# Kernel tuning notes

Hardware: AMD Instinct MI355X
Metric: run time of the kernel (lower is better)

## Reference

```python
import jax, jax.numpy as jnp
import numpy as np
from jax import lax

BOS, EOS = 62, 63
NEG_BIG = -10000.0


def setup_inputs() -> dict:
    key = jax.random.key(0)
    k_em, k_tag, k_len, k_tr = jax.random.split(key, 4)
    B, S, L = 512, 1024, 64
    emissions = jax.random.normal(k_em, (B, S, L), dtype=jnp.float32)
    tags = jax.random.randint(k_tag, (B, S), 0, 62).astype(jnp.int64)
    # valid-prefix mask from random lengths in [S//2, S]
    lengths = jax.random.randint(k_len, (B,), S // 2, S + 1)
    mask = (jnp.arange(S)[None, :] < lengths[:, None]).astype(jnp.float32)
    # transitions: uniform(-0.1, 0.1) with BOS/EOS constraints as in init_weights
    transitions = jax.random.uniform(k_tr, (L, L), minval=-0.1, maxval=0.1, dtype=jnp.float32)
    transitions = transitions.at[:, BOS].set(NEG_BIG)
    transitions = transitions.at[EOS, :].set(NEG_BIG)
    return {"emissions": emissions, "tags": tags, "mask": mask, "transitions": transitions}


def _crf_nll(emissions, tags, mask, transitions):
    B, S, L = emissions.shape
    # ----- gold-path scores -----
    first_tags = tags[:, 0]
    last_idx = (mask.sum(axis=1).astype(jnp.int32) - 1)  # (B,)
    last_tags = jnp.take_along_axis(tags, last_idx[:, None].astype(tags.dtype), axis=1)[:, 0]
    scores = transitions[BOS, first_tags]
    scores = scores + jnp.take_along_axis(emissions[:, 0], first_tags[:, None], axis=1)[:, 0]
    prev_t, cur_t = tags[:, :-1], tags[:, 1:]
    e_step = jnp.take_along_axis(emissions[:, 1:], cur_t[..., None], axis=-1)[..., 0]  # (B,S-1)
    t_step = transitions[prev_t, cur_t]  # (B,S-1)
    scores = scores + jnp.sum((e_step + t_step) * mask[:, 1:], axis=1)
    scores = scores + transitions[last_tags, EOS]
    # ----- log-partition via forward algorithm -----
    alpha0 = transitions[BOS][None, :] + emissions[:, 0]  # (B,L)
    em_t = jnp.moveaxis(emissions[:, 1:], 1, 0)  # (S-1,B,L)
    mk_t = mask[:, 1:].T  # (S-1,B)

    def step(alpha, xs):
        e_t, m_t = xs
        # alpha[b,i] + T[i,j] + e_t[b,j] -> logsumexp over i
        new = jax.nn.logsumexp(alpha[:, :, None] + transitions[None, :, :] + e_t[:, None, :], axis=1)
        return jnp.where(m_t[:, None] > 0, new, alpha), None

    alpha, _ = lax.scan(step, alpha0, (em_t, mk_t))
    partition = jax.nn.logsumexp(alpha + transitions[:, EOS][None, :], axis=1)  # (B,)
    return -jnp.sum(scores - partition)


def reference(emissions, tags, mask, transitions):
    return _crf_nll(emissions, tags, mask, transitions)
```

## Files before the change

kernel.cpp:

```cpp
#include <hip/hip_runtime.h>
#include <math.h>

#define BOS_TAG 62
#define EOS_TAG 63
#define S_LEN   1024
#define NCH     32
#define CH      32
#define WPB     2
#define LN2F    0.69314718055994530942f

typedef short  short8 __attribute__((ext_vector_type(8)));
typedef float  f32x4  __attribute__((ext_vector_type(4)));

template <int CTRL>
__device__ __forceinline__ int dpp_mov(int v) {
  return __builtin_amdgcn_update_dpp(v, v, CTRL, 0xf, 0xf, false);
}
template <int CTRL>
__device__ __forceinline__ float dpp_fmax_step(float v) {
  return fmaxf(v, __int_as_float(dpp_mov<CTRL>(__float_as_int(v))));
}
__device__ __forceinline__ float wave_fmax_all(float v) {
  v = dpp_fmax_step<0x111>(v); v = dpp_fmax_step<0x112>(v);
  v = dpp_fmax_step<0x114>(v); v = dpp_fmax_step<0x118>(v);
  v = dpp_fmax_step<0x142>(v); v = dpp_fmax_step<0x143>(v);
  return __int_as_float(__builtin_amdgcn_readlane(__float_as_int(v), 63));
}
template <int CTRL>
__device__ __forceinline__ float dpp_fadd_step(float v) {
  int t = __builtin_amdgcn_update_dpp(0, __float_as_int(v), CTRL, 0xf, 0xf, true);
  return v + __int_as_float(t);
}
__device__ __forceinline__ float wave_sum_all(float v) {
  v = dpp_fadd_step<0x111>(v); v = dpp_fadd_step<0x112>(v);
  v = dpp_fadd_step<0x114>(v); v = dpp_fadd_step<0x118>(v);
  v = dpp_fadd_step<0x142>(v); v = dpp_fadd_step<0x143>(v);
  return __int_as_float(__builtin_amdgcn_readlane(__float_as_int(v), 63));
}
__device__ __forceinline__ unsigned short f2bf(float v) {
  return (unsigned short)((__float_as_uint(v) + 0x8000u) >> 16);
}
__device__ __forceinline__ float bf2f(unsigned short u) {
  return __uint_as_float(((unsigned)u) << 16);
}

__global__ __launch_bounds__(256) void crf_lens(
    const float* __restrict__ mask, int* __restrict__ lens, int B)
{
  const int b = blockIdx.x * 4 + (threadIdx.x >> 6);
  if (b >= B) return;
  const int l = threadIdx.x & 63;
  const float4* mb = (const float4*)(mask + (size_t)b * S_LEN);
  float s = 0.f;
#pragma unroll
  for (int i = 0; i < 4; ++i) { float4 q = mb[l + 64 * i]; s += q.x + q.y + q.z + q.w; }
  s = wave_sum_all(s);
  if (l == 0) lens[b] = max(1, min(S_LEN, (int)(s + 0.5f)));
}

__global__ __launch_bounds__(256) void crf_ptab(
    const float* __restrict__ trans, short8* __restrict__ pfrag,
    float* __restrict__ tvf)
{
  const int tid = threadIdx.x;
  for (int e = tid; e < 1024; e += 256) {
    int lane = e & 63, kc = (e >> 6) & 1, m = (e >> 7) & 3, dir = e >> 9;
    int g = lane >> 4, c = lane & 15;
    int out = 16 * m + c;
    short8 f;
#pragma unroll
    for (int j = 0; j < 8; ++j) {
      int in = 16 * (2 * kc + (j >> 2)) + 4 * g + (j & 3);
      float tv = dir ? trans[out * 64 + in] : trans[in * 64 + out];
      f[j] = (short)f2bf(__expf(tv));
    }
    pfrag[e] = f;
  }
  if (tid < 64) tvf[tid] = __expf(trans[tid * 64 + EOS_TAG]);
}

__global__ __launch_bounds__(256, 2) void crf_chunk_mfma(
    const float* __restrict__ em, const float* __restrict__ trans,
    const int* __restrict__ lens, const short8* __restrict__ pfrag,
    unsigned short* __restrict__ Vf, unsigned short* __restrict__ Vb,
    float* __restrict__ sf, float* __restrict__ sb,
    float* __restrict__ m0a, int B)
{
  const int l  = threadIdx.x & 63;
  const int w  = blockIdx.x * 4 + (threadIdx.x >> 6);
  const int nwaves = 2 * B * WPB;
  if (w >= nwaves) return;
  const int dir  = w & 1;
  const int idx  = w >> 1;
  const int b    = idx / WPB;
  const int half = idx % WPB;
  const float* embase = em + (size_t)b * S_LEN * 64;
  const int g = l >> 4, c = l & 15;

  const int len = lens[b];

  float m0 = 0.f;
  if (dir == 0 && half == 0) {
    float a0 = trans[BOS_TAG * 64 + l] + embase[l];
    m0 = wave_fmax_all(a0);
    if (l == 0) m0a[b] = m0;
  }

  unsigned short* Vout = dir ? Vb : Vf;
  float* sout = dir ? sb : sf;
  int ps = -1, pr = -1;
#pragma unroll
  for (int r = 0; r < 16; ++r) {
    int kg = half * 16 + r;
    int fs = min((kg + 1) * CH, len - 1) - (kg * CH + 1);
    if (fs < 0) {
      Vout[((size_t)b * NCH + kg) * 64 + l] = 0x3F80;
      if (l == 0) sout[b * NCH + kg] = 0.f;
    }
    if (fs >= 0 && fs < CH - 1) { ps = fs; pr = r; }
  }

  if (half * 16 * CH + 1 > len - 1) return;

  short8 Af[4][2];
#pragma unroll
  for (int m = 0; m < 4; ++m)
#pragma unroll
    for (int kc = 0; kc < 2; ++kc)
      Af[m][kc] = pfrag[((dir * 4 + m) * 2 + kc) * 64 + l];

  float d[4][4];
#pragma unroll
  for (int m = 0; m < 4; ++m)
#pragma unroll
    for (int r = 0; r < 4; ++r) d[m][r] = 1.0f;
  if (dir == 0 && half == 0 && c == 0) {
#pragma unroll
    for (int m = 0; m < 4; ++m) {
      float4 tq = *reinterpret_cast<const float4*>(trans + BOS_TAG * 64 + 16 * m + 4 * g);
      float4 eq = *reinterpret_cast<const float4*>(embase + 16 * m + 4 * g);
      d[m][0] = __expf(tq.x + eq.x - m0);
      d[m][1] = __expf(tq.y + eq.y - m0);
      d[m][2] = __expf(tq.z + eq.z - m0);
      d[m][3] = __expf(tq.w + eq.w - m0);
    }
  }

  int sigma = 0;
  auto renorm16 = [&]() {
    float mx = d[0][0];
#pragma unroll
    for (int m = 0; m < 4; ++m)
#pragma unroll
      for (int r = 0; r < 4; ++r) mx = fmaxf(mx, d[m][r]);
    mx = wave_fmax_all(mx);
    int e = ((__float_as_int(mx) >> 23) & 0xff) - 127;
    float s = __int_as_float((127 - e) << 23);
#pragma unroll
    for (int m = 0; m < 4; ++m)
#pragma unroll
      for (int r = 0; r < 4; ++r) d[m][r] *= s;
    sigma += e;
  };
  auto save_chain = [&](int r) {
    int kg = half * 16 + r;
    if (c == r) {
      unsigned short* dst = Vout + ((size_t)b * NCH + kg) * 64;
#pragma unroll
      for (int m = 0; m < 4; ++m) {
        uint2 val;
        val.x = (unsigned)f2bf(d[m][0]) | ((unsigned)f2bf(d[m][1]) << 16);
        val.y = (unsigned)f2bf(d[m][2]) | ((unsigned)f2bf(d[m][3]) << 16);
        *reinterpret_cast<uint2*>(dst + 16 * m + 4 * g) = val;
      }
    }
    if (l == r) sout[b * NCH + kg] = (float)sigma;
  };

  const int tb0c  = (half * 16 + c) * CH + 1;
  const int tendc = min((half * 16 + c + 1) * CH, len - 1);
  auto loadE = [&](float4* q, int tl) {
    int tr = dir ? max(tendc - tl, 0) : min(tb0c + tl, S_LEN - 1);
    const float* rowp = embase + (size_t)tr * 64 + 4 * g;
    q[0] = *reinterpret_cast<const float4*>(rowp);
    q[1] = *reinterpret_cast<const float4*>(rowp + 16);
    q[2] = *reinterpret_cast<const float4*>(rowp + 32);
    q[3] = *reinterpret_cast<const float4*>(rowp + 48);
  };

  auto mfma8 = [&](const short8& bv0, const short8& bv1, f32x4* acc) {
#pragma unroll
    for (int m = 0; m < 4; ++m) {
      f32x4 z = {0.f, 0.f, 0.f, 0.f};
      z = __builtin_amdgcn_mfma_f32_16x16x32_bf16(Af[m][0], bv0, z, 0, 0, 0);
      acc[m] = __builtin_amdgcn_mfma_f32_16x16x32_bf16(Af[m][1], bv1, z, 0, 0, 0);
    }
  };

  auto bodyF = [&](const float4* q, int tl, bool rn) {
    short8 bv0, bv1;
#pragma unroll
    for (int j = 0; j < 8; ++j) {
      bv0[j] = (short)f2bf(d[(j >> 2)][j & 3]);
      bv1[j] = (short)f2bf(d[2 + (j >> 2)][j & 3]);
    }
    f32x4 acc[4];
    mfma8(bv0, bv1, acc);
#pragma unroll
    for (int m = 0; m < 4; ++m) {
      d[m][0] = acc[m][0] * __expf(q[m].x);
      d[m][1] = acc[m][1] * __expf(q[m].y);
      d[m][2] = acc[m][2] * __expf(q[m].z);
      d[m][3] = acc[m][3] * __expf(q[m].w);
    }
    if (rn) renorm16();
    if (tl == ps) save_chain(pr);
  };
  auto bodyB = [&](const float4* q, int tl, bool rn) {
    float ex[4][4];
#pragma unroll
    for (int m = 0; m < 4; ++m) {
      ex[m][0] = __expf(q[m].x); ex[m][1] = __expf(q[m].y);
      ex[m][2] = __expf(q[m].z); ex[m][3] = __expf(q[m].w);
    }
    short8 bv0, bv1;
#pragma unroll
    for (int j = 0; j < 8; ++j) {
      bv0[j] = (short)f2bf(d[(j >> 2)][j & 3] * ex[(j >> 2)][j & 3]);
      bv1[j] = (short)f2bf(d[2 + (j >> 2)][j & 3] * ex[2 + (j >> 2)][j & 3]);
    }
    f32x4 acc[4];
    mfma8(bv0, bv1, acc);
#pragma unroll
    for (int m = 0; m < 4; ++m) {
      d[m][0] = acc[m][0]; d[m][1] = acc[m][1];
      d[m][2] = acc[m][2]; d[m][3] = acc[m][3];
    }
    if (rn) renorm16();
    if (tl == ps) save_chain(pr);
  };

  float4 p0[4], p1[4], p2[4], p3[4];
  loadE(p0, 0); loadE(p1, 1); loadE(p2, 2); loadE(p3, 3);
  if (dir == 0) {
#pragma unroll 1
    for (int t4 = 0; t4 < CH; t4 += 4) {
      bodyF(p0, t4 + 0, false); loadE(p0, t4 + 4);
      bodyF(p1, t4 + 1, false); loadE(p1, t4 + 5);
      bodyF(p2, t4 + 2, false); loadE(p2, t4 + 6);
      bodyF(p3, t4 + 3, true);  loadE(p3, t4 + 7);
    }
  } else {
#pragma unroll 1
    for (int t4 = 0; t4 < CH; t4 += 4) {
      bodyB(p0, t4 + 0, false); loadE(p0, t4 + 4);
      bodyB(p1, t4 + 1, false); loadE(p1, t4 + 5);
      bodyB(p2, t4 + 2, false); loadE(p2, t4 + 6);
      bodyB(p3, t4 + 3, true);  loadE(p3, t4 + 7);
    }
  }

  {
    int kg = half * 16 + c;
    bool full = (kg + 1) * CH <= len - 1;
    if (full) {
      unsigned short* dst = Vout + ((size_t)b * NCH + kg) * 64;
#pragma unroll
      for (int m = 0; m < 4; ++m) {
        uint2 val;
        val.x = (unsigned)f2bf(d[m][0]) | ((unsigned)f2bf(d[m][1]) << 16);
        val.y = (unsigned)f2bf(d[m][2]) | ((unsigned)f2bf(d[m][3]) << 16);
        *reinterpret_cast<uint2*>(dst + 16 * m + 4 * g) = val;
      }
    }
    if (l < 16 && (half * 16 + l + 1) * CH <= len - 1)
      sout[b * NCH + half * 16 + l] = (float)sigma;
  }
}

__global__ __launch_bounds__(256) void crf_combine(
    const float* __restrict__ em, const int* __restrict__ tags,
    const float* __restrict__ trans, const int* __restrict__ lens,
    const unsigned short* __restrict__ Vf, const unsigned short* __restrict__ Vb,
    const float* __restrict__ sf, const float* __restrict__ sb,
    const float* __restrict__ m0a, const float* __restrict__ tvf,
    float* __restrict__ term, int B)
{
  const int item = blockIdx.x * 4 + (threadIdx.x >> 6);
  if (item >= B * NCH) return;
  const int b = item / NCH, k = item - b * NCH;
  const int l = threadIdx.x & 63;
  const int len = lens[b];
  const int kb = (len >= 2) ? (len - 2) / CH : 0;

  const int* tb = tags + (size_t)b * S_LEN;
  const float* emb = em + (size_t)b * S_LEN * 64;

  float t = 0.f;
  {
    float sc = 0.f;
    int t0 = k * CH + 1 + l;
    if (l < CH && t0 <= len - 1) {
      int cur = tb[t0], prev = tb[t0 - 1];
      sc = emb[(size_t)t0 * 64 + cur] + trans[prev * 64 + cur];
    }
    if (k == 0) {
      if (l == 32) sc += trans[BOS_TAG * 64 + tb[0]] + emb[tb[0]];
      if (l == 33) sc += trans[tb[len - 1] * 64 + EOS_TAG];
    }
    t -= wave_sum_all(sc);
  }

  const unsigned short* vf = Vf + ((size_t)b * NCH + k) * 64;
  if (k == 0) {
    float v0 = bf2f(vf[l]);
    if (kb == 0) {
      t += m0a[b] + LN2F * sf[b * NCH] + __logf(wave_sum_all(v0 * tvf[l]));
    } else {
      t += m0a[b] + LN2F * (sf[b * NCH] + sb[b * NCH + 1])
         + __logf(wave_sum_all(v0 * bf2f(Vb[((size_t)b * NCH + 1) * 64 + l])));
    }
  } else if (k < kb) {
    float vk = bf2f(vf[l]);
    t += LN2F * sb[b * NCH + k + 1]
       + __logf(wave_sum_all(vk * bf2f(Vb[((size_t)b * NCH + k + 1) * 64 + l])))
       - __logf(wave_sum_all(vk));
  } else if (k == kb) {
    float vk = bf2f(vf[l]);
    t += __logf(wave_sum_all(vk * tvf[l])) - __logf(wave_sum_all(vk));
  }

  if (l == 0) term[item] = t;
}

__global__ __launch_bounds__(1024) void crf_final(
    const float* __restrict__ term, float* __restrict__ out, int n)
{
  __shared__ float red[16];
  float s = 0.f;
  for (int i = threadIdx.x; i < n; i += 1024) s += term[i];
  s = wave_sum_all(s);
  const int wid = threadIdx.x >> 6;
  if ((threadIdx.x & 63) == 0) red[wid] = s;
  __syncthreads();
  if (threadIdx.x == 0) {
    float tot = 0.f;
#pragma unroll
    for (int i = 0; i < 16; ++i) tot += red[i];
    out[0] = tot;
  }
}

__global__ __launch_bounds__(64) void crf_mono(
    const float* __restrict__ em, const int* __restrict__ tags,
    const float* __restrict__ mask, const float* __restrict__ trans,
    float* __restrict__ partial)
{
  const int b = blockIdx.x;
  const int l = threadIdx.x;
  const float* emb = em + (size_t)b * S_LEN * 64;
  const float* mb = mask + (size_t)b * S_LEN;
  float lenf = 0.f;
  for (int t = l; t < S_LEN; t += 64) lenf += mb[t];
  lenf = wave_sum_all(lenf);
  const int len = max(1, min(S_LEN, (int)(lenf + 0.5f)));

  float p[64];
#pragma unroll
  for (int i = 0; i < 64; ++i) p[i] = __expf(trans[i * 64 + l]) * 0.015625f;

  const int* tb = tags + (size_t)b * S_LEN;
  float sc = 0.f;
  for (int tt = 1 + l; tt <= len - 1; tt += 64)
    sc += emb[(size_t)tt * 64 + tb[tt]] + trans[tb[tt - 1] * 64 + tb[tt]];
  sc = wave_sum_all(sc);
  sc += trans[BOS_TAG * 64 + tb[0]] + emb[tb[0]] + trans[tb[len - 1] * 64 + EOS_TAG];

  float a0 = trans[BOS_TAG * 64 + l] + emb[l];
  float m0 = wave_fmax_all(a0);
  float v = __expf(a0 - m0);
  int sigma = 0;
  for (int t = 1; t <= len - 1; ++t) {
    float E = __expf(emb[(size_t)t * 64 + l]);
    int xi = __float_as_int(v);
    float s0 = 0.f, s1 = 0.f, s2 = 0.f, s3 = 0.f;
#pragma unroll
    for (int i = 0; i < 64; i += 4) {
      s0 = fmaf(__int_as_float(__builtin_amdgcn_readlane(xi, i + 0)), p[i + 0], s0);
      s1 = fmaf(__int_as_float(__builtin_amdgcn_readlane(xi, i + 1)), p[i + 1], s1);
      s2 = fmaf(__int_as_float(__builtin_amdgcn_readlane(xi, i + 2)), p[i + 2], s2);
      s3 = fmaf(__int_as_float(__builtin_amdgcn_readlane(xi, i + 3)), p[i + 3], s3);
    }
    v = ((s0 + s1) + (s2 + s3)) * E;
    float m = wave_fmax_all(v);
    int e = ((__float_as_int(m) >> 23) & 0xff) - 127;
    sigma += e + 6;
    v *= __int_as_float((127 - e) << 23);
  }
  float tvec = __expf(trans[l * 64 + EOS_TAG]);
  float lp = m0 + LN2F * (float)sigma + __logf(wave_sum_all(v * tvec));
  if (l == 0) partial[b] = lp - sc;
}

extern "C" void kernel_launch(void* const* d_in, const int* in_sizes, int n_in,
                              void* d_out, int out_size, void* d_ws, size_t ws_size,
                              hipStream_t stream) {
  const float* em = (const float*)d_in[0];
  const int* tags = (const int*)d_in[1];
  const float* mask = (const float*)d_in[2];
  const float* trans = (const float*)d_in[3];
  float* out = (float*)d_out;

  const int B = in_sizes[1] / S_LEN;

  const size_t nSig = (size_t)B * NCH;
  const size_t nV   = (size_t)B * NCH * 64;
  const size_t need = 16384 + 64 * sizeof(float)
                    + (3 * nSig + (size_t)B) * sizeof(float)
                    + (size_t)B * sizeof(int)
                    + 2 * nV * sizeof(unsigned short);

  if (ws_size >= need) {
    short8* pfrag = (short8*)d_ws;
    float* tvf  = (float*)((char*)d_ws + 16384);
    float* sf   = tvf + 64;
    float* sb   = sf + nSig;
    float* m0a  = sb + nSig;
    float* term = m0a + B;
    int*   lens = (int*)(term + nSig);
    unsigned short* Vf = (unsigned short*)(lens + B);
    unsigned short* Vb = Vf + nV;

    crf_lens<<<(B + 3) / 4, 256, 0, stream>>>(mask, lens, B);
    crf_ptab<<<1, 256, 0, stream>>>(trans, pfrag, tvf);
    const int nwaves = 2 * B * WPB;
    crf_chunk_mfma<<<(nwaves + 3) / 4, 256, 0, stream>>>(
        em, trans, lens, pfrag, Vf, Vb, sf, sb, m0a, B);
    crf_combine<<<(B * NCH + 3) / 4, 256, 0, stream>>>(
        em, tags, trans, lens, Vf, Vb, sf, sb, m0a, tvf, term, B);
    crf_final<<<1, 1024, 0, stream>>>(term, out, B * NCH);
  } else {
    float* partial = (float*)d_ws;
    crf_mono<<<B, 64, 0, stream>>>(em, tags, mask, trans, partial);
    crf_final<<<1, 1024, 0, stream>>>(partial, out, B);
  }
}
```

Before: 72.52 us.

## Use 64-step chunks, merge prep kernels, and replace final reduction with atomics

Doubles the chunk length to 64 and halves the chunk count to 16, so each batch row now has one wave per direction instead of two. The lens and transition-table kernels are merged into a single prep kernel that also zeroes the output. The separate final reduction kernel is replaced by atomicAdd from the combine kernel. Together this removes two launches and halves the combine work, but the scan kernel has half as many waves with longer serial chains and less parallelism.

```diff
diff --git a/kernel.cpp b/kernel.cpp
--- a/kernel.cpp
+++ b/kernel.cpp
@@ -4,9 +4,9 @@
 #define BOS_TAG 62
 #define EOS_TAG 63
 #define S_LEN   1024
-#define NCH     32
-#define CH      32
-#define WPB     2
+#define NCH     16
+#define CH      64
+#define WPB     1
 #define LN2F    0.69314718055994530942f
 
 typedef short  short8 __attribute__((ext_vector_type(8)));
@@ -44,39 +44,39 @@
   return __uint_as_float(((unsigned)u) << 16);
 }
 
-__global__ __launch_bounds__(256) void crf_lens(
-    const float* __restrict__ mask, int* __restrict__ lens, int B)
-{
-  const int b = blockIdx.x * 4 + (threadIdx.x >> 6);
-  if (b >= B) return;
-  const int l = threadIdx.x & 63;
-  const float4* mb = (const float4*)(mask + (size_t)b * S_LEN);
-  float s = 0.f;
-#pragma unroll
-  for (int i = 0; i < 4; ++i) { float4 q = mb[l + 64 * i]; s += q.x + q.y + q.z + q.w; }
-  s = wave_sum_all(s);
-  if (l == 0) lens[b] = max(1, min(S_LEN, (int)(s + 0.5f)));
-}
-
-__global__ __launch_bounds__(256) void crf_ptab(
-    const float* __restrict__ trans, short8* __restrict__ pfrag,
-    float* __restrict__ tvf)
+__global__ __launch_bounds__(256) void crf_prep(
+    const float* __restrict__ mask, const float* __restrict__ trans,
+    int* __restrict__ lens, short8* __restrict__ pfrag,
+    float* __restrict__ tvf, float* __restrict__ out, int B)
 {
   const int tid = threadIdx.x;
-  for (int e = tid; e < 1024; e += 256) {
-    int lane = e & 63, kc = (e >> 6) & 1, m = (e >> 7) & 3, dir = e >> 9;
-    int g = lane >> 4, c = lane & 15;
-    int out = 16 * m + c;
-    short8 f;
-#pragma unroll
-    for (int j = 0; j < 8; ++j) {
-      int in = 16 * (2 * kc + (j >> 2)) + 4 * g + (j & 3);
-      float tv = dir ? trans[out * 64 + in] : trans[in * 64 + out];
-      f[j] = (short)f2bf(__expf(tv));
-    }
-    pfrag[e] = f;
-  }
-  if (tid < 64) tvf[tid] = __expf(trans[tid * 64 + EOS_TAG]);
+  const int b = blockIdx.x * 4 + (tid >> 6);
+  if (b < B) {
+    const int l = tid & 63;
+    const float4* mb = (const float4*)(mask + (size_t)b * S_LEN);
+    float s = 0.f;
+#pragma unroll
+    for (int i = 0; i < 4; ++i) { float4 q = mb[l + 64 * i]; s += q.x + q.y + q.z + q.w; }
+    s = wave_sum_all(s);
+    if (l == 0) lens[b] = max(1, min(S_LEN, (int)(s + 0.5f)));
+  }
+  if (blockIdx.x == 0) {
+    for (int e = tid; e < 1024; e += 256) {
+      int lane = e & 63, kc = (e >> 6) & 1, m = (e >> 7) & 3, dir = e >> 9;
+      int g = lane >> 4, c = lane & 15;
+      int out_s = 16 * m + c;
+      short8 f;
+#pragma unroll
+      for (int j = 0; j < 8; ++j) {
+        int in_s = 16 * (2 * kc + (j >> 2)) + 4 * g + (j & 3);
+        float tv = dir ? trans[out_s * 64 + in_s] : trans[in_s * 64 + out_s];
+        f[j] = (short)f2bf(__expf(tv));
+      }
+      pfrag[e] = f;
+    }
+    if (tid < 64) tvf[tid] = __expf(trans[tid * 64 + EOS_TAG]);
+    if (tid == 0) out[0] = 0.f;
+  }
 }
 
 __global__ __launch_bounds__(256, 2) void crf_chunk_mfma(
@@ -91,16 +91,15 @@
   const int nwaves = 2 * B * WPB;
   if (w >= nwaves) return;
   const int dir  = w & 1;
-  const int idx  = w >> 1;
-  const int b    = idx / WPB;
-  const int half = idx % WPB;
+  const int b    = w >> 1;
+  const int half = 0;
   const float* embase = em + (size_t)b * S_LEN * 64;
   const int g = l >> 4, c = l & 15;
 
   const int len = lens[b];
 
   float m0 = 0.f;
-  if (dir == 0 && half == 0) {
+  if (dir == 0) {
     float a0 = trans[BOS_TAG * 64 + l] + embase[l];
     m0 = wave_fmax_all(a0);
     if (l == 0) m0a[b] = m0;
@@ -120,7 +119,6 @@
     if (fs >= 0 && fs < CH - 1) { ps = fs; pr = r; }
   }
 
-  if (half * 16 * CH + 1 > len - 1) return;
 
   short8 Af[4][2];
 #pragma unroll
@@ -134,7 +132,7 @@
   for (int m = 0; m < 4; ++m)
 #pragma unroll
     for (int r = 0; r < 4; ++r) d[m][r] = 1.0f;
-  if (dir == 0 && half == 0 && c == 0) {
+  if (dir == 0 && c == 0) {
 #pragma unroll
     for (int m = 0; m < 4; ++m) {
       float4 tq = *reinterpret_cast<const float4*>(trans + BOS_TAG * 64 + 16 * m + 4 * g);
@@ -284,7 +282,7 @@
     const unsigned short* __restrict__ Vf, const unsigned short* __restrict__ Vb,
     const float* __restrict__ sf, const float* __restrict__ sb,
     const float* __restrict__ m0a, const float* __restrict__ tvf,
-    float* __restrict__ term, int B)
+    float* __restrict__ out, int B)
 {
   const int item = blockIdx.x * 4 + (threadIdx.x >> 6);
   if (item >= B * NCH) return;
@@ -300,13 +298,15 @@
   {
     float sc = 0.f;
     int t0 = k * CH + 1 + l;
-    if (l < CH && t0 <= len - 1) {
+    if (t0 <= min((k + 1) * CH, len - 1)) {
       int cur = tb[t0], prev = tb[t0 - 1];
       sc = emb[(size_t)t0 * 64 + cur] + trans[prev * 64 + cur];
     }
     if (k == 0) {
-      if (l == 32) sc += trans[BOS_TAG * 64 + tb[0]] + emb[tb[0]];
-      if (l == 33) sc += trans[tb[len - 1] * 64 + EOS_TAG];
+      if (l == 32 || (l == 33)) {
+        sc += (l == 32) ? (trans[BOS_TAG * 64 + tb[0]] + emb[tb[0]])
+                        : trans[tb[len - 1] * 64 + EOS_TAG];
+      }
     }
     t -= wave_sum_all(sc);
   }
@@ -330,25 +330,7 @@
     t += __logf(wave_sum_all(vk * tvf[l])) - __logf(wave_sum_all(vk));
   }
 
-  if (l == 0) term[item] = t;
-}
-
-__global__ __launch_bounds__(1024) void crf_final(
-    const float* __restrict__ term, float* __restrict__ out, int n)
-{
-  __shared__ float red[16];
-  float s = 0.f;
-  for (int i = threadIdx.x; i < n; i += 1024) s += term[i];
-  s = wave_sum_all(s);
-  const int wid = threadIdx.x >> 6;
-  if ((threadIdx.x & 63) == 0) red[wid] = s;
-  __syncthreads();
-  if (threadIdx.x == 0) {
-    float tot = 0.f;
-#pragma unroll
-    for (int i = 0; i < 16; ++i) tot += red[i];
-    out[0] = tot;
-  }
+  if (l == 0) atomicAdd(out, t);
 }
 
 __global__ __launch_bounds__(64) void crf_mono(
@@ -402,6 +384,24 @@
   if (l == 0) partial[b] = lp - sc;
 }
 
+__global__ __launch_bounds__(1024) void crf_final(
+    const float* __restrict__ term, float* __restrict__ out, int n)
+{
+  __shared__ float red[16];
+  float s = 0.f;
+  for (int i = threadIdx.x; i < n; i += 1024) s += term[i];
+  s = wave_sum_all(s);
+  const int wid = threadIdx.x >> 6;
+  if ((threadIdx.x & 63) == 0) red[wid] = s;
+  __syncthreads();
+  if (threadIdx.x == 0) {
+    float tot = 0.f;
+#pragma unroll
+    for (int i = 0; i < 16; ++i) tot += red[i];
+    out[0] = tot;
+  }
+}
+
 extern "C" void kernel_launch(void* const* d_in, const int* in_sizes, int n_in,
                               void* d_out, int out_size, void* d_ws, size_t ws_size,
                               hipStream_t stream) {
@@ -416,7 +416,7 @@
   const size_t nSig = (size_t)B * NCH;
   const size_t nV   = (size_t)B * NCH * 64;
   const size_t need = 16384 + 64 * sizeof(float)
-                    + (3 * nSig + (size_t)B) * sizeof(float)
+                    + (2 * nSig + (size_t)B) * sizeof(float)
                     + (size_t)B * sizeof(int)
                     + 2 * nV * sizeof(unsigned short);
 
@@ -426,19 +426,16 @@
     float* sf   = tvf + 64;
     float* sb   = sf + nSig;
     float* m0a  = sb + nSig;
-    float* term = m0a + B;
-    int*   lens = (int*)(term + nSig);
+    int*   lens = (int*)(m0a + B);
     unsigned short* Vf = (unsigned short*)(lens + B);
     unsigned short* Vb = Vf + nV;
 
-    crf_lens<<<(B + 3) / 4, 256, 0, stream>>>(mask, lens, B);
-    crf_ptab<<<1, 256, 0, stream>>>(trans, pfrag, tvf);
+    crf_prep<<<(B + 3) / 4, 256, 0, stream>>>(mask, trans, lens, pfrag, tvf, out, B);
     const int nwaves = 2 * B * WPB;
     crf_chunk_mfma<<<(nwaves + 3) / 4, 256, 0, stream>>>(
         em, trans, lens, pfrag, Vf, Vb, sf, sb, m0a, B);
     crf_combine<<<(B * NCH + 3) / 4, 256, 0, stream>>>(
-        em, tags, trans, lens, Vf, Vb, sf, sb, m0a, tvf, term, B);
-    crf_final<<<1, 1024, 0, stream>>>(term, out, B * NCH);
+        em, tags, trans, lens, Vf, Vb, sf, sb, m0a, tvf, out, B);
   } else {
     float* partial = (float*)d_ws;
     crf_mono<<<B, 64, 0, stream>>>(em, tags, mask, trans, partial);
```

Result: slower. 155.7 us (+114.7%).
